# Kernel tuning notes

Measured on AMD Instinct MI355X. Metric: run time of the kernel, lower is better.

## Reference

```python
import jax, jax.numpy as jnp
import numpy as np

N_EMBD = 384
N_HEAD = 6
HEAD_SIZE = N_EMBD // N_HEAD  # 64
B, T = 128, 256
EPS = 1e-5


def setup_inputs() -> dict:
    key = jax.random.key(0)
    ks = jax.random.split(key, 12)
    s = 0.02
    return {
        "x": jax.random.normal(ks[0], (B, T, N_EMBD), dtype=jnp.float32),
        "Wk": jax.random.normal(ks[1], (N_EMBD, N_EMBD), dtype=jnp.float32) * s,
        "Wq": jax.random.normal(ks[2], (N_EMBD, N_EMBD), dtype=jnp.float32) * s,
        "Wv": jax.random.normal(ks[3], (N_EMBD, N_EMBD), dtype=jnp.float32) * s,
        "Wo": jax.random.normal(ks[4], (N_EMBD, N_EMBD), dtype=jnp.float32) * s,
        "bo": jnp.zeros((N_EMBD,), dtype=jnp.float32),
        "W1": jax.random.normal(ks[5], (N_EMBD, 4 * N_EMBD), dtype=jnp.float32) * s,
        "b1": jnp.zeros((4 * N_EMBD,), dtype=jnp.float32),
        "W2": jax.random.normal(ks[6], (4 * N_EMBD, N_EMBD), dtype=jnp.float32) * s,
        "b2": jnp.zeros((N_EMBD,), dtype=jnp.float32),
        "g1": jnp.ones((N_EMBD,), dtype=jnp.float32),
        "be1": jnp.zeros((N_EMBD,), dtype=jnp.float32),
        "g2": jnp.ones((N_EMBD,), dtype=jnp.float32),
        "be2": jnp.zeros((N_EMBD,), dtype=jnp.float32),
    }


def _layernorm(x, g, b):
    mu = jnp.mean(x, axis=-1, keepdims=True)
    var = jnp.var(x, axis=-1, keepdims=True)
    return (x - mu) * jax.lax.rsqrt(var + EPS) * g + b


def _attention(x, Wk, Wq, Wv, Wo, bo):
    Bb, Tt, C = x.shape
    H, D = N_HEAD, HEAD_SIZE
    k = (x @ Wk).reshape(Bb, Tt, H, D).transpose(0, 2, 1, 3)  # (B,H,T,D)
    q = (x @ Wq).reshape(Bb, Tt, H, D).transpose(0, 2, 1, 3)
    v = (x @ Wv).reshape(Bb, Tt, H, D).transpose(0, 2, 1, 3)
    wei = jnp.einsum("bhqd,bhkd->bhqk", q, k) * (D ** -0.5)  # (B,H,T,T)
    mask = jnp.tril(jnp.ones((Tt, Tt), dtype=bool))
    wei = jnp.where(mask, wei, -jnp.inf)
    wei = jax.nn.softmax(wei, axis=-1)
    out = jnp.einsum("bhqk,bhkd->bhqd", wei, v)
    out = out.transpose(0, 2, 1, 3).reshape(Bb, Tt, H * D)
    return out @ Wo + bo


def reference(x, Wk, Wq, Wv, Wo, bo, W1, b1, W2, b2, g1, be1, g2, be2):
    # dropout is identity in eval mode
    h = _layernorm(x, g1, be1)
    x = x + _attention(h, Wk, Wq, Wv, Wo, bo)
    h = _layernorm(x, g2, be2)
    ff = jax.nn.relu(h @ W1 + b1) @ W2 + b2
    return x + ff
```

## Files before the change

### kernel.cpp

```cpp
#include <hip/hip_runtime.h>

typedef unsigned short u16;
typedef short s16x8 __attribute__((ext_vector_type(8)));
typedef float f32x4 __attribute__((ext_vector_type(4)));

__device__ inline u16 f2bf(float f) {
    unsigned u = __float_as_uint(f);
    u += 0x7FFF + ((u >> 16) & 1);
    return (u16)(u >> 16);
}
__device__ inline float bf2f(u16 h) {
    return __uint_as_float((unsigned)h << 16);
}

__device__ inline f32x4 mfma16(s16x8 a, s16x8 b, f32x4 c) {
    return __builtin_amdgcn_mfma_f32_16x16x32_bf16(a, b, c, 0, 0, 0);
}

__device__ __forceinline__ void gl16(const u16* g, u16* l) {
    __builtin_amdgcn_global_load_lds(
        (const __attribute__((address_space(1))) void*)g,
        (__attribute__((address_space(3))) void*)l, 16, 0, 0);
}

__global__ void tcvt_all(const float* __restrict__ Wq, const float* __restrict__ Wk,
                         const float* __restrict__ Wv, const float* __restrict__ Wo,
                         const float* __restrict__ W1, const float* __restrict__ W2,
                         u16* __restrict__ out) {
    int i = blockIdx.x * 256 + threadIdx.x;
    float val;
    if (i < 589824) {
        int q = i / 147456, j = i - q * 147456;
        const float* s = q == 0 ? Wq : q == 1 ? Wk : q == 2 ? Wv : Wo;
        int n = j / 384, k = j - n * 384;
        val = s[k * 384 + n];
    } else if (i < 1179648) {
        int j = i - 589824;
        int n = j / 384, k = j - n * 384;
        val = W1[(size_t)k * 1536 + n];
    } else {
        int j = i - 1179648;
        int n = j / 1536, k = j - n * 1536;
        val = W2[(size_t)k * 384 + n];
    }
    out[i] = f2bf(val);
}

__global__ __launch_bounds__(256) void ln_kernel(const float* __restrict__ x,
                                                 const float* __restrict__ g,
                                                 const float* __restrict__ be,
                                                 u16* __restrict__ out) {
    int lane = threadIdx.x & 63;
    int w = threadIdx.x >> 6;
    int row = blockIdx.x * 4 + w;
    const float* xr = x + (size_t)row * 384;
    float v[6];
    float s = 0.f, sq = 0.f;
#pragma unroll
    for (int i = 0; i < 6; ++i) {
        v[i] = xr[i * 64 + lane];
        s += v[i];
        sq += v[i] * v[i];
    }
#pragma unroll
    for (int m = 1; m < 64; m <<= 1) {
        s += __shfl_xor(s, m);
        sq += __shfl_xor(sq, m);
    }
    float mu = s * (1.0f / 384.0f);
    float var = sq * (1.0f / 384.0f) - mu * mu;
    float rstd = rsqrtf(var + 1e-5f);
    u16* orow = out + (size_t)row * 384;
#pragma unroll
    for (int i = 0; i < 6; ++i) {
        int col = i * 64 + lane;
        orow[col] = f2bf((v[i] - mu) * rstd * g[col] + be[col]);
    }
}

__global__ __launch_bounds__(256) void ln_bf16_kernel(const u16* __restrict__ x,
                                                      const float* __restrict__ g,
                                                      const float* __restrict__ be,
                                                      u16* __restrict__ out) {
    int lane = threadIdx.x & 63;
    int w = threadIdx.x >> 6;
    int row = blockIdx.x * 4 + w;
    const u16* xr = x + (size_t)row * 384;
    bool act = lane < 48;
    float v[8];
    float s = 0.f, sq = 0.f;
    if (act) {
        s16x8 t = *(const s16x8*)&xr[lane * 8];
#pragma unroll
        for (int j = 0; j < 8; ++j) {
            v[j] = bf2f((u16)t[j]);
            s += v[j];
            sq += v[j] * v[j];
        }
    }
#pragma unroll
    for (int m = 1; m < 64; m <<= 1) {
        s += __shfl_xor(s, m);
        sq += __shfl_xor(sq, m);
    }
    float mu = s * (1.0f / 384.0f);
    float var = sq * (1.0f / 384.0f) - mu * mu;
    float rstd = rsqrtf(var + 1e-5f);
    if (act) {
        float4 g0 = *(const float4*)&g[lane * 8];
        float4 g1 = *(const float4*)&g[lane * 8 + 4];
        float4 b0 = *(const float4*)&be[lane * 8];
        float4 b1 = *(const float4*)&be[lane * 8 + 4];
        float gg[8] = {g0.x, g0.y, g0.z, g0.w, g1.x, g1.y, g1.z, g1.w};
        float bb[8] = {b0.x, b0.y, b0.z, b0.w, b1.x, b1.y, b1.z, b1.w};
        u16* orow = out + (size_t)row * 384 + lane * 8;
#pragma unroll
        for (int j = 0; j < 8; ++j)
            orow[j] = f2bf((v[j] - mu) * rstd * gg[j] + bb[j]);
    }
}

template <int BIAS, int RELU, int RES, int RESBF, int OBF16, int NBX>
__global__ __launch_bounds__(256) void gemm_kernel(const u16* __restrict__ A,
                                                   const u16* __restrict__ Bt,
                                                   const float* __restrict__ bias,
                                                   const void* __restrict__ res,
                                                   void* __restrict__ out,
                                                   int M, int N, int K) {
    __shared__ u16 La[2][128 * 32];
    __shared__ u16 Lb[2][128 * 32];
    int tid = threadIdx.x;
    int lane = tid & 63, w = tid >> 6;
    int wm = w >> 1, wn = w & 1;
    int lr = lane & 15, lg = lane >> 4;

    int nwg = gridDim.x;
    int q = nwg >> 3, r = nwg & 7;
    int xcd = blockIdx.x & 7, lin = blockIdx.x >> 3;
    int wg = (xcd < r ? xcd * (q + 1) : r * (q + 1) + (xcd - r) * q) + lin;
    int bx = wg % NBX, by = wg / NBX;
    int m0 = by * 128, n0 = bx * 128;

    int gslot = ((lane & 3) ^ ((lane >> 3) & 3)) * 8;
    const u16* pa[2];
    const u16* pb[2];
#pragma unroll
    for (int i = 0; i < 2; ++i) {
        int rr = w * 32 + i * 16 + (lane >> 2);
        pa[i] = A + (size_t)(m0 + rr) * K + gslot;
        pb[i] = Bt + (size_t)(n0 + rr) * K + gslot;
    }

    f32x4 acc[4][4];
    f32x4 zero = {0.f, 0.f, 0.f, 0.f};
#pragma unroll
    for (int mt = 0; mt < 4; ++mt)
#pragma unroll
        for (int nt = 0; nt < 4; ++nt) acc[mt][nt] = zero;

    int sel = (lg ^ ((lr >> 1) & 3)) << 3;
    int nt_steps = K >> 5;

    {
        u16* la = La[0] + w * 32 * 32;
        u16* lb = Lb[0] + w * 32 * 32;
        gl16(pa[0], la);
        gl16(pa[1], la + 16 * 32);
        gl16(pb[0], lb);
        gl16(pb[1], lb + 16 * 32);
    }

    for (int t = 0; t < nt_steps; ++t) {
        asm volatile("s_waitcnt vmcnt(0)" ::: "memory");
        __builtin_amdgcn_s_barrier();
        asm volatile("" ::: "memory");
        if (t + 1 < nt_steps) {
            int kc = (t + 1) << 5;
            u16* la = La[(t + 1) & 1] + w * 32 * 32;
            u16* lb = Lb[(t + 1) & 1] + w * 32 * 32;
            gl16(pa[0] + kc, la);
            gl16(pa[1] + kc, la + 16 * 32);
            gl16(pb[0] + kc, lb);
            gl16(pb[1] + kc, lb + 16 * 32);
        }
        const u16* lab = La[t & 1];
        const u16* lbb = Lb[t & 1];
        s16x8 af[4], bfr[4];
#pragma unroll
        for (int tt = 0; tt < 4; ++tt) {
            int mr = wm * 64 + tt * 16 + lr;
            int nr = wn * 64 + tt * 16 + lr;
            af[tt] = *(const s16x8*)&lab[mr * 32 + sel];
            bfr[tt] = *(const s16x8*)&lbb[nr * 32 + sel];
        }
#pragma unroll
        for (int mt = 0; mt < 4; ++mt)
#pragma unroll
            for (int nt = 0; nt < 4; ++nt)
                acc[mt][nt] = mfma16(af[mt], bfr[nt], acc[mt][nt]);
    }

#pragma unroll
    for (int mt = 0; mt < 4; ++mt) {
#pragma unroll
        for (int nt = 0; nt < 4; ++nt) {
            int m_base = m0 + wm * 64 + mt * 16 + lg * 4;
            int n = n0 + wn * 64 + nt * 16 + lr;
            float bv = BIAS ? bias[n] : 0.0f;
#pragma unroll
            for (int r2 = 0; r2 < 4; ++r2) {
                size_t idx = (size_t)(m_base + r2) * N + n;
                float val = acc[mt][nt][r2] + bv;
                if (RES) {
                    if (RESBF)
                        val += bf2f(((const u16*)res)[idx]);
                    else
                        val += ((const float*)res)[idx];
                }
                if (RELU) val = fmaxf(val, 0.0f);
                if (OBF16)
                    ((u16*)out)[idx] = f2bf(val);
                else
                    ((float*)out)[idx] = val;
            }
        }
    }
}

__global__ __launch_bounds__(512) void attn_kernel(const u16* __restrict__ qkv,
                                                   u16* __restrict__ aout) {
    __shared__ u16 Kl[256 * 72];
    __shared__ u16 Vt[64 * 264];
    __shared__ u16 Pl[8 * 16 * 264];
    int qt = blockIdx.x, h = blockIdx.y, b = blockIdx.z;
    int tid = threadIdx.x, lane = tid & 63, w = tid >> 6;
    int lr = lane & 15, lg = lane >> 4;
    const u16* qb = qkv + (size_t)b * 256 * 1152;

#pragma unroll
    for (int i = 0; i < 4; ++i) {
        int c = tid + i * 512;
        int t = c >> 3, dch = c & 7;
        *(int4*)&Kl[t * 72 + dch * 8] =
            *(const int4*)(qb + (size_t)t * 1152 + 384 + h * 64 + dch * 8);
        union { int4 v; u16 u[8]; } vv;
        vv.v = *(const int4*)(qb + (size_t)t * 1152 + 768 + h * 64 + dch * 8);
#pragma unroll
        for (int j = 0; j < 8; ++j) Vt[(dch * 8 + j) * 264 + t] = vv.u[j];
    }

    int q0 = qt * 128;
    const u16* qrow = qb + (size_t)(q0 + w * 16 + lr) * 1152 + h * 64;
    s16x8 qf0 = *(const s16x8*)(qrow + lg * 8);
    s16x8 qf1 = *(const s16x8*)(qrow + 32 + lg * 8);

    __syncthreads();

    f32x4 zero = {0.f, 0.f, 0.f, 0.f};
    f32x4 s[16];
#pragma unroll
    for (int nt = 0; nt < 16; ++nt) s[nt] = zero;
#pragma unroll
    for (int nt = 0; nt < 16; ++nt) {
        s16x8 kf0 = *(const s16x8*)&Kl[(nt * 16 + lr) * 72 + lg * 8];
        s16x8 kf1 = *(const s16x8*)&Kl[(nt * 16 + lr) * 72 + 32 + lg * 8];
        s[nt] = mfma16(qf0, kf0, s[nt]);
        s[nt] = mfma16(qf1, kf1, s[nt]);
    }

    int ib = q0 + w * 16 + lg * 4;
    float mx[4] = {-1e30f, -1e30f, -1e30f, -1e30f};
#pragma unroll
    for (int nt = 0; nt < 16; ++nt) {
        int jg = nt * 16 + lr;
#pragma unroll
        for (int r = 0; r < 4; ++r) {
            float val = s[nt][r] * 0.125f;
            val = (jg <= ib + r) ? val : -1e30f;
            s[nt][r] = val;
            mx[r] = fmaxf(mx[r], val);
        }
    }
#pragma unroll
    for (int r = 0; r < 4; ++r) {
        mx[r] = fmaxf(mx[r], __shfl_xor(mx[r], 1));
        mx[r] = fmaxf(mx[r], __shfl_xor(mx[r], 2));
        mx[r] = fmaxf(mx[r], __shfl_xor(mx[r], 4));
        mx[r] = fmaxf(mx[r], __shfl_xor(mx[r], 8));
    }
    float rs[4] = {0.f, 0.f, 0.f, 0.f};
#pragma unroll
    for (int nt = 0; nt < 16; ++nt) {
#pragma unroll
        for (int r = 0; r < 4; ++r) {
            float p = __expf(s[nt][r] - mx[r]);
            s[nt][r] = p;
            rs[r] += p;
        }
    }
#pragma unroll
    for (int r = 0; r < 4; ++r) {
        rs[r] += __shfl_xor(rs[r], 1);
        rs[r] += __shfl_xor(rs[r], 2);
        rs[r] += __shfl_xor(rs[r], 4);
        rs[r] += __shfl_xor(rs[r], 8);
    }
    u16* Pw = &Pl[w * 16 * 264];
#pragma unroll
    for (int nt = 0; nt < 16; ++nt)
#pragma unroll
        for (int r = 0; r < 4; ++r)
            Pw[(lg * 4 + r) * 264 + nt * 16 + lr] = f2bf(s[nt][r]);

    __syncthreads();

    f32x4 o[4];
#pragma unroll
    for (int nt = 0; nt < 4; ++nt) o[nt] = zero;
#pragma unroll
    for (int kc = 0; kc < 8; ++kc) {
        s16x8 pf = *(const s16x8*)&Pw[lr * 264 + kc * 32 + lg * 8];
#pragma unroll
        for (int nt = 0; nt < 4; ++nt) {
            s16x8 vf = *(const s16x8*)&Vt[(nt * 16 + lr) * 264 + kc * 32 + lg * 8];
            o[nt] = mfma16(pf, vf, o[nt]);
        }
    }
    float inv[4];
#pragma unroll
    for (int r = 0; r < 4; ++r) inv[r] = 1.0f / rs[r];
    u16* ob = aout + (size_t)(b * 256 + q0 + w * 16) * 384 + h * 64;
#pragma unroll
    for (int nt = 0; nt < 4; ++nt)
#pragma unroll
        for (int r = 0; r < 4; ++r)
            ob[(size_t)(lg * 4 + r) * 384 + nt * 16 + lr] = f2bf(o[nt][r] * inv[r]);
}

extern "C" void kernel_launch(void* const* d_in, const int* in_sizes, int n_in,
                              void* d_out, int out_size, void* d_ws, size_t ws_size,
                              hipStream_t stream) {
    const float* x   = (const float*)d_in[0];
    const float* Wk  = (const float*)d_in[1];
    const float* Wq  = (const float*)d_in[2];
    const float* Wv  = (const float*)d_in[3];
    const float* Wo  = (const float*)d_in[4];
    const float* bo  = (const float*)d_in[5];
    const float* W1  = (const float*)d_in[6];
    const float* b1  = (const float*)d_in[7];
    const float* W2  = (const float*)d_in[8];
    const float* b2  = (const float*)d_in[9];
    const float* g1  = (const float*)d_in[10];
    const float* be1 = (const float*)d_in[11];
    const float* g2  = (const float*)d_in[12];
    const float* be2 = (const float*)d_in[13];

    char* ws = (char*)d_ws;
    u16* hbuf = (u16*)(ws + 0);
    u16* qkv  = (u16*)(ws + 25165824);
    u16* ao   = (u16*)(ws + 100663296);
    u16* x1   = (u16*)(ws + 125829120);
    u16* ubuf = (u16*)(ws + 25165824);
    u16* wT   = (u16*)(ws + 150994944);
    u16* wqkvT = wT;
    u16* woT   = wT + 442368;
    u16* w1T   = woT + 147456;
    u16* w2T   = w1T + 589824;

    tcvt_all<<<6912, 256, 0, stream>>>(Wq, Wk, Wv, Wo, W1, W2, wT);

    ln_kernel<<<8192, 256, 0, stream>>>(x, g1, be1, hbuf);
    gemm_kernel<0, 0, 0, 0, 1, 9><<<2304, 256, 0, stream>>>(
        hbuf, wqkvT, nullptr, nullptr, qkv, 32768, 1152, 384);
    attn_kernel<<<dim3(2, 6, 128), 512, 0, stream>>>(qkv, ao);
    gemm_kernel<1, 0, 1, 0, 1, 3><<<768, 256, 0, stream>>>(
        ao, woT, bo, x, x1, 32768, 384, 384);
    ln_bf16_kernel<<<8192, 256, 0, stream>>>(x1, g2, be2, hbuf);
    gemm_kernel<1, 1, 0, 0, 1, 12><<<3072, 256, 0, stream>>>(
        hbuf, w1T, b1, nullptr, ubuf, 32768, 1536, 384);
    gemm_kernel<1, 0, 1, 1, 0, 3><<<768, 256, 0, stream>>>(
        ubuf, w2T, b2, x1, (float*)d_out, 32768, 384, 1536);
}
```

Measured before the change: 288.5 us.

## Enlarge GEMM tiles to 256x192x64 with 8 waves and XOR-swizzled LDS

Measured after the change: 262.6 us. 1.1x faster.

```diff
diff --git a/kernel.cpp b/kernel.cpp
--- a/kernel.cpp
+++ b/kernel.cpp
@@ -120,15 +120,15 @@
     }
 }
 
-template <int BIAS, int RELU, int RES, int RESBF, int OBF16, int NBX>
-__global__ __launch_bounds__(256) void gemm_kernel(const u16* __restrict__ A,
-                                                   const u16* __restrict__ Bt,
-                                                   const float* __restrict__ bias,
-                                                   const void* __restrict__ res,
-                                                   void* __restrict__ out,
-                                                   int M, int N, int K) {
-    __shared__ u16 La[2][128 * 32];
-    __shared__ u16 Lb[2][128 * 32];
+template <int BIAS, int RELU, int RES, int RESBF, int OBF16, int NBN>
+__global__ __launch_bounds__(512, 2) void gemm_kernel(const u16* __restrict__ A,
+                                                      const u16* __restrict__ Bt,
+                                                      const float* __restrict__ bias,
+                                                      const void* __restrict__ res,
+                                                      void* __restrict__ out,
+                                                      int M, int N, int K) {
+    __shared__ u16 La[2][256 * 64];
+    __shared__ u16 Lb[2][192 * 64];
     int tid = threadIdx.x;
     int lane = tid & 63, w = tid >> 6;
     int wm = w >> 1, wn = w & 1;
@@ -138,74 +138,80 @@
     int q = nwg >> 3, r = nwg & 7;
     int xcd = blockIdx.x & 7, lin = blockIdx.x >> 3;
     int wg = (xcd < r ? xcd * (q + 1) : r * (q + 1) + (xcd - r) * q) + lin;
-    int bx = wg % NBX, by = wg / NBX;
-    int m0 = by * 128, n0 = bx * 128;
-
-    int gslot = ((lane & 3) ^ ((lane >> 3) & 3)) * 8;
-    const u16* pa[2];
-    const u16* pb[2];
-#pragma unroll
-    for (int i = 0; i < 2; ++i) {
-        int rr = w * 32 + i * 16 + (lane >> 2);
-        pa[i] = A + (size_t)(m0 + rr) * K + gslot;
-        pb[i] = Bt + (size_t)(n0 + rr) * K + gslot;
-    }
-
-    f32x4 acc[4][4];
+    int bx = wg % NBN, by = wg / NBN;
+    int m0 = by * 256, n0 = bx * 192;
+
+    int rsub = lane >> 3;
+    int gslot = ((lane & 7) ^ rsub) * 8;
+    const u16* pa[4];
+    const u16* pb[3];
+#pragma unroll
+    for (int i = 0; i < 4; ++i)
+        pa[i] = A + (size_t)(m0 + w * 32 + i * 8 + rsub) * K + gslot;
+#pragma unroll
+    for (int i = 0; i < 3; ++i)
+        pb[i] = Bt + (size_t)(n0 + w * 24 + i * 8 + rsub) * K + gslot;
+
+    f32x4 acc[4][6];
     f32x4 zero = {0.f, 0.f, 0.f, 0.f};
 #pragma unroll
     for (int mt = 0; mt < 4; ++mt)
 #pragma unroll
-        for (int nt = 0; nt < 4; ++nt) acc[mt][nt] = zero;
-
-    int sel = (lg ^ ((lr >> 1) & 3)) << 3;
-    int nt_steps = K >> 5;
-
-    {
-        u16* la = La[0] + w * 32 * 32;
-        u16* lb = Lb[0] + w * 32 * 32;
-        gl16(pa[0], la);
-        gl16(pa[1], la + 16 * 32);
-        gl16(pb[0], lb);
-        gl16(pb[1], lb + 16 * 32);
-    }
+        for (int nt = 0; nt < 6; ++nt) acc[mt][nt] = zero;
+
+    int s0 = (lg ^ (lr & 7)) * 8;
+    int s1 = ((4 + lg) ^ (lr & 7)) * 8;
+    int nt_steps = K >> 6;
+
+#define STAGE(t, bsel)                                        \
+    do {                                                      \
+        int kc = (t) << 6;                                    \
+        _Pragma("unroll")                                     \
+        for (int i = 0; i < 4; ++i)                           \
+            gl16(pa[i] + kc, &La[bsel][(w * 32 + i * 8) * 64]); \
+        _Pragma("unroll")                                     \
+        for (int i = 0; i < 3; ++i)                           \
+            gl16(pb[i] + kc, &Lb[bsel][(w * 24 + i * 8) * 64]); \
+    } while (0)
+
+    STAGE(0, 0);
 
     for (int t = 0; t < nt_steps; ++t) {
         asm volatile("s_waitcnt vmcnt(0)" ::: "memory");
         __builtin_amdgcn_s_barrier();
         asm volatile("" ::: "memory");
-        if (t + 1 < nt_steps) {
-            int kc = (t + 1) << 5;
-            u16* la = La[(t + 1) & 1] + w * 32 * 32;
-            u16* lb = Lb[(t + 1) & 1] + w * 32 * 32;
-            gl16(pa[0] + kc, la);
-            gl16(pa[1] + kc, la + 16 * 32);
-            gl16(pb[0] + kc, lb);
-            gl16(pb[1] + kc, lb + 16 * 32);
-        }
+        if (t + 1 < nt_steps) STAGE(t + 1, (t + 1) & 1);
         const u16* lab = La[t & 1];
         const u16* lbb = Lb[t & 1];
-        s16x8 af[4], bfr[4];
-#pragma unroll
-        for (int tt = 0; tt < 4; ++tt) {
-            int mr = wm * 64 + tt * 16 + lr;
-            int nr = wn * 64 + tt * 16 + lr;
-            af[tt] = *(const s16x8*)&lab[mr * 32 + sel];
-            bfr[tt] = *(const s16x8*)&lbb[nr * 32 + sel];
-        }
-#pragma unroll
-        for (int mt = 0; mt < 4; ++mt)
-#pragma unroll
-            for (int nt = 0; nt < 4; ++nt)
-                acc[mt][nt] = mfma16(af[mt], bfr[nt], acc[mt][nt]);
-    }
+        s16x8 af[2][4], bfr[2][6];
+#pragma unroll
+        for (int mt = 0; mt < 4; ++mt) {
+            int mr = wm * 64 + mt * 16 + lr;
+            af[0][mt] = *(const s16x8*)&lab[mr * 64 + s0];
+            af[1][mt] = *(const s16x8*)&lab[mr * 64 + s1];
+        }
+#pragma unroll
+        for (int nt = 0; nt < 6; ++nt) {
+            int nr = wn * 96 + nt * 16 + lr;
+            bfr[0][nt] = *(const s16x8*)&lbb[nr * 64 + s0];
+            bfr[1][nt] = *(const s16x8*)&lbb[nr * 64 + s1];
+        }
+#pragma unroll
+        for (int kk = 0; kk < 2; ++kk)
+#pragma unroll
+            for (int mt = 0; mt < 4; ++mt)
+#pragma unroll
+                for (int nt = 0; nt < 6; ++nt)
+                    acc[mt][nt] = mfma16(af[kk][mt], bfr[kk][nt], acc[mt][nt]);
+    }
+#undef STAGE
 
 #pragma unroll
     for (int mt = 0; mt < 4; ++mt) {
 #pragma unroll
-        for (int nt = 0; nt < 4; ++nt) {
+        for (int nt = 0; nt < 6; ++nt) {
             int m_base = m0 + wm * 64 + mt * 16 + lg * 4;
-            int n = n0 + wn * 64 + nt * 16 + lr;
+            int n = n0 + wn * 96 + nt * 16 + lr;
             float bv = BIAS ? bias[n] : 0.0f;
 #pragma unroll
             for (int r2 = 0; r2 < 4; ++r2) {
@@ -370,14 +376,14 @@
     tcvt_all<<<6912, 256, 0, stream>>>(Wq, Wk, Wv, Wo, W1, W2, wT);
 
     ln_kernel<<<8192, 256, 0, stream>>>(x, g1, be1, hbuf);
-    gemm_kernel<0, 0, 0, 0, 1, 9><<<2304, 256, 0, stream>>>(
+    gemm_kernel<0, 0, 0, 0, 1, 6><<<768, 512, 0, stream>>>(
         hbuf, wqkvT, nullptr, nullptr, qkv, 32768, 1152, 384);
     attn_kernel<<<dim3(2, 6, 128), 512, 0, stream>>>(qkv, ao);
-    gemm_kernel<1, 0, 1, 0, 1, 3><<<768, 256, 0, stream>>>(
+    gemm_kernel<1, 0, 1, 0, 1, 2><<<256, 512, 0, stream>>>(
         ao, woT, bo, x, x1, 32768, 384, 384);
     ln_bf16_kernel<<<8192, 256, 0, stream>>>(x1, g2, be2, hbuf);
-    gemm_kernel<1, 1, 0, 0, 1, 12><<<3072, 256, 0, stream>>>(
+    gemm_kernel<1, 1, 0, 0, 1, 8><<<1024, 512, 0, stream>>>(
         hbuf, w1T, b1, nullptr, ubuf, 32768, 1536, 384);
-    gemm_kernel<1, 0, 1, 1, 0, 3><<<768, 256, 0, stream>>>(
+    gemm_kernel<1, 0, 1, 1, 0, 2><<<256, 512, 0, stream>>>(
         ubuf, w2T, b2, x1, (float*)d_out, 32768, 384, 1536);
 }
```
